# Kernel optimization log

Measured on AMD Instinct MI355X. Metric: run time of the kernel, lower is better.

Reference implementation:

```python
import jax, jax.numpy as jnp
import numpy as np


def setup_inputs() -> dict:
    key = jax.random.key(0)
    k1, k2 = jax.random.split(key)
    B, C, H, W = 64, 512, 28, 28
    x = jax.random.normal(k1, (B, C, H, W), dtype=jnp.float32)
    cc = jax.random.randint(k2, (B, H, W), 0, 2).astype(jnp.bool_)
    return {"x": x, "cc": cc}


def reference(x, cc):
    # x: [B, C, H, W], cc: [B, H, W] bool mask
    m = cc.astype(x.dtype)
    # ave_pool: tmp initialized to x[:, :, 0, 0], then accumulates masked positions
    masked_sum = jnp.einsum('bchw,bhw->bc', x, m) + x[:, :, 0, 0]  # [B, C]
    cnt = jnp.sum(m, axis=(1, 2))                                   # [B]
    denom = jnp.where(cnt == 0, jnp.ones_like(cnt), cnt)            # count==0 -> no division
    mean_pool = masked_sum / denom[:, None]                         # [B, C]
    # AdaptiveMaxPool2d(1): global spatial max
    max_pool = jnp.max(x, axis=(2, 3))                              # [B, C]
    return jnp.concatenate([mean_pool, max_pool], axis=1)           # [B, 2C]
```

## Files before the change

### kernel.cpp

```cpp
#include <hip/hip_runtime.h>


#define HW   784
#define NV4  196
#define NC   512
#define NB   64

__global__ __launch_bounds__(256) void mask_prep_kernel(
    const void* __restrict__ cc, float* __restrict__ mask_f,
    float* __restrict__ invd)
{
    __shared__ float s_cnt;
    __shared__ int s_bad_int, s_bad_flt;
    const int b = blockIdx.x;
    const int t = threadIdx.x;
    if (t == 0) { s_cnt = 0.0f; s_bad_int = 0; s_bad_flt = 0; }
    __syncthreads();

    const int* cci = (const int*)cc;
    if (t < NV4) {
        int v = cci[b * NV4 + t];
        if (v & ~1) atomicOr(&s_bad_int, 1);
        if (v != 0 && v != 0x3F800000) atomicOr(&s_bad_flt, 1);
    }
    __syncthreads();

    float local = 0.0f;
    if (s_bad_int == 0) {
        const int* row = cci + (size_t)b * HW;
        for (int i = t; i < HW; i += 256) {
            float mv = (float)row[i];
            mask_f[b * HW + i] = mv; local += mv;
        }
    } else if (s_bad_flt == 0) {
        const float* row = (const float*)cc + (size_t)b * HW;
        for (int i = t; i < HW; i += 256) {
            float mv = row[i];
            mask_f[b * HW + i] = mv; local += mv;
        }
    } else {
        const unsigned char* row = (const unsigned char*)cc + (size_t)b * HW;
        for (int i = t; i < HW; i += 256) {
            float mv = (float)row[i];
            mask_f[b * HW + i] = mv; local += mv;
        }
    }
    atomicAdd(&s_cnt, local);
    __syncthreads();
    if (t == 0) {
        float c = s_cnt;
        invd[b] = 1.0f / ((c == 0.0f) ? 1.0f : c);
    }
}

__device__ __forceinline__ float dot4(float4 a, float4 b) {
    return a.x * b.x + a.y * b.y + a.z * b.z + a.w * b.w;
}
__device__ __forceinline__ float max4(float4 a) {
    return fmaxf(fmaxf(a.x, a.y), fmaxf(a.z, a.w));
}

__global__ __launch_bounds__(256) void pool_main_kernel(
    const float* __restrict__ x, const float* __restrict__ mask_f,
    const float* __restrict__ invd, float* __restrict__ out)
{
    const int blk  = blockIdx.x;
    const int b    = blk >> 5;
    const int grp  = blk & 31;
    const int t    = threadIdx.x;
    const int wave = t >> 6;
    const int lane = t & 63;
    const int c0   = grp * 16 + wave * 4;

    const float4* m4 = (const float4*)(mask_f + (size_t)b * HW);
    float4 m0 = m4[lane];
    float4 m1 = m4[lane + 64];
    float4 m2 = m4[lane + 128];
    float4 m3 = (lane < 4) ? m4[lane + 192] : make_float4(0.f, 0.f, 0.f, 0.f);
    const float inv = invd[b];

    float s[4], mx[4];
#pragma unroll
    for (int j = 0; j < 4; ++j) {
        const float4* xr = (const float4*)(x + (size_t)(b * NC + c0 + j) * HW);
        float4 q0 = xr[lane];
        float4 q1 = xr[lane + 64];
        float4 q2 = xr[lane + 128];
        float sum = dot4(q0, m0) + dot4(q1, m1) + dot4(q2, m2);
        float mm  = fmaxf(fmaxf(max4(q0), max4(q1)), max4(q2));
        if (lane < 4) {
            float4 q3 = xr[lane + 192];
            sum += dot4(q3, m3);
            mm = fmaxf(mm, max4(q3));
        }
        if (lane == 0) sum += q0.x;
        s[j] = sum; mx[j] = mm;
    }

#pragma unroll
    for (int j = 0; j < 4; ++j) {
        float sum = s[j], mm = mx[j];
        for (int off = 32; off > 0; off >>= 1) {
            sum += __shfl_down(sum, off);
            mm   = fmaxf(mm, __shfl_down(mm, off));
        }
        if (lane == 0) {
            const int c = c0 + j;
            out[(size_t)b * (2 * NC) + c]      = sum * inv;
            out[(size_t)b * (2 * NC) + NC + c] = mm;
        }
    }
}

extern "C" void kernel_launch(void* const* d_in, const int* in_sizes, int n_in,
                              void* d_out, int out_size, void* d_ws, size_t ws_size,
                              hipStream_t stream) {
    const float* x  = (const float*)d_in[0];
    const void*  cc = d_in[1];
    float* out    = (float*)d_out;
    float* mask_f = (float*)d_ws;
    float* invd   = (float*)d_ws + (size_t)NB * HW;

    mask_prep_kernel<<<dim3(NB), dim3(256), 0, stream>>>(cc, mask_f, invd);
    pool_main_kernel<<<dim3(NB * 32), dim3(256), 0, stream>>>(x, mask_f, invd, out);
}
```

Baseline: 155.6 us.

## Fuse mask preparation into pooling kernel and drop separate prep launch

Removes the mask_prep kernel and its workspace round trip. Each wave of the pooling kernel now detects the mask dtype, loads and converts the mask itself, and computes the count and reciprocal locally. The count reduction is interleaved with the per-channel sum and max reductions in one shuffle loop. This removes one launch and the dependency between two kernels, at the cost of every wave redundantly reading and converting the mask.

```diff
diff --git a/kernel.cpp b/kernel.cpp
--- a/kernel.cpp
+++ b/kernel.cpp
@@ -1,57 +1,9 @@
 #include <hip/hip_runtime.h>
 
 
-#define HW   784
-#define NV4  196
-#define NC   512
-#define NB   64
-
-__global__ __launch_bounds__(256) void mask_prep_kernel(
-    const void* __restrict__ cc, float* __restrict__ mask_f,
-    float* __restrict__ invd)
-{
-    __shared__ float s_cnt;
-    __shared__ int s_bad_int, s_bad_flt;
-    const int b = blockIdx.x;
-    const int t = threadIdx.x;
-    if (t == 0) { s_cnt = 0.0f; s_bad_int = 0; s_bad_flt = 0; }
-    __syncthreads();
-
-    const int* cci = (const int*)cc;
-    if (t < NV4) {
-        int v = cci[b * NV4 + t];
-        if (v & ~1) atomicOr(&s_bad_int, 1);
-        if (v != 0 && v != 0x3F800000) atomicOr(&s_bad_flt, 1);
-    }
-    __syncthreads();
-
-    float local = 0.0f;
-    if (s_bad_int == 0) {
-        const int* row = cci + (size_t)b * HW;
-        for (int i = t; i < HW; i += 256) {
-            float mv = (float)row[i];
-            mask_f[b * HW + i] = mv; local += mv;
-        }
-    } else if (s_bad_flt == 0) {
-        const float* row = (const float*)cc + (size_t)b * HW;
-        for (int i = t; i < HW; i += 256) {
-            float mv = row[i];
-            mask_f[b * HW + i] = mv; local += mv;
-        }
-    } else {
-        const unsigned char* row = (const unsigned char*)cc + (size_t)b * HW;
-        for (int i = t; i < HW; i += 256) {
-            float mv = (float)row[i];
-            mask_f[b * HW + i] = mv; local += mv;
-        }
-    }
-    atomicAdd(&s_cnt, local);
-    __syncthreads();
-    if (t == 0) {
-        float c = s_cnt;
-        invd[b] = 1.0f / ((c == 0.0f) ? 1.0f : c);
-    }
-}
+#define HW 784
+#define NC 512
+#define NB 64
 
 __device__ __forceinline__ float dot4(float4 a, float4 b) {
     return a.x * b.x + a.y * b.y + a.z * b.z + a.w * b.w;
@@ -59,10 +11,17 @@
 __device__ __forceinline__ float max4(float4 a) {
     return fmaxf(fmaxf(a.x, a.y), fmaxf(a.z, a.w));
 }
+__device__ __forceinline__ float sum4(float4 a) {
+    return a.x + a.y + a.z + a.w;
+}
+__device__ __forceinline__ float4 unpack_u8(unsigned int u) {
+    return make_float4((float)(u & 0xff), (float)((u >> 8) & 0xff),
+                       (float)((u >> 16) & 0xff), (float)((u >> 24) & 0xff));
+}
 
-__global__ __launch_bounds__(256) void pool_main_kernel(
-    const float* __restrict__ x, const float* __restrict__ mask_f,
-    const float* __restrict__ invd, float* __restrict__ out)
+__global__ __launch_bounds__(256) void pool_fused_kernel(
+    const float* __restrict__ x, const void* __restrict__ cc,
+    float* __restrict__ out)
 {
     const int blk  = blockIdx.x;
     const int b    = blk >> 5;
@@ -72,12 +31,44 @@
     const int lane = t & 63;
     const int c0   = grp * 16 + wave * 4;
 
-    const float4* m4 = (const float4*)(mask_f + (size_t)b * HW);
-    float4 m0 = m4[lane];
-    float4 m1 = m4[lane + 64];
-    float4 m2 = m4[lane + 128];
-    float4 m3 = (lane < 4) ? m4[lane + 192] : make_float4(0.f, 0.f, 0.f, 0.f);
-    const float inv = invd[b];
+    int badInt = 0, badFlt = 0;
+    {
+        const int4* det = (const int4*)((const unsigned char*)cc + (size_t)b * HW);
+        if (lane < 49) {
+            int4 d = det[lane];
+            badInt = (d.x | d.y | d.z | d.w) & ~1;
+            badFlt = (d.x && d.x != 0x3F800000) || (d.y && d.y != 0x3F800000) ||
+                     (d.z && d.z != 0x3F800000) || (d.w && d.w != 0x3F800000);
+        }
+    }
+    const bool isInt = !__any(badInt != 0);
+    const bool isFlt = !__any(badFlt);
+
+    float4 m0, m1, m2, m3 = make_float4(0.f, 0.f, 0.f, 0.f);
+    if (isInt) {
+        const int4* mi = (const int4*)cc + (size_t)b * 196;
+        int4 a = mi[lane], e = mi[lane + 64], f = mi[lane + 128];
+        m0 = make_float4((float)a.x, (float)a.y, (float)a.z, (float)a.w);
+        m1 = make_float4((float)e.x, (float)e.y, (float)e.z, (float)e.w);
+        m2 = make_float4((float)f.x, (float)f.y, (float)f.z, (float)f.w);
+        if (lane < 4) {
+            int4 g = mi[lane + 192];
+            m3 = make_float4((float)g.x, (float)g.y, (float)g.z, (float)g.w);
+        }
+    } else if (isFlt) {
+        const float4* mf = (const float4*)cc + (size_t)b * 196;
+        m0 = mf[lane]; m1 = mf[lane + 64]; m2 = mf[lane + 128];
+        if (lane < 4) m3 = mf[lane + 192];
+    } else {
+        const unsigned int* row =
+            (const unsigned int*)((const unsigned char*)cc + (size_t)b * HW);
+        m0 = unpack_u8(row[lane]);
+        m1 = unpack_u8(row[lane + 64]);
+        m2 = unpack_u8(row[lane + 128]);
+        if (lane < 4) m3 = unpack_u8(row[lane + 192]);
+    }
+
+    float mc = sum4(m0) + sum4(m1) + sum4(m2) + sum4(m3);
 
     float s[4], mx[4];
 #pragma unroll
@@ -97,17 +88,22 @@
         s[j] = sum; mx[j] = mm;
     }
 
+    for (int off = 32; off > 0; off >>= 1) {
+        mc += __shfl_down(mc, off);
 #pragma unroll
-    for (int j = 0; j < 4; ++j) {
-        float sum = s[j], mm = mx[j];
-        for (int off = 32; off > 0; off >>= 1) {
-            sum += __shfl_down(sum, off);
-            mm   = fmaxf(mm, __shfl_down(mm, off));
+        for (int j = 0; j < 4; ++j) {
+            s[j] += __shfl_down(s[j], off);
+            mx[j] = fmaxf(mx[j], __shfl_down(mx[j], off));
         }
-        if (lane == 0) {
+    }
+
+    if (lane == 0) {
+        const float inv = 1.0f / ((mc == 0.0f) ? 1.0f : mc);
+#pragma unroll
+        for (int j = 0; j < 4; ++j) {
             const int c = c0 + j;
-            out[(size_t)b * (2 * NC) + c]      = sum * inv;
-            out[(size_t)b * (2 * NC) + NC + c] = mm;
+            out[(size_t)b * (2 * NC) + c]      = s[j] * inv;
+            out[(size_t)b * (2 * NC) + NC + c] = mx[j];
         }
     }
 }
@@ -117,10 +113,6 @@
                               hipStream_t stream) {
     const float* x  = (const float*)d_in[0];
     const void*  cc = d_in[1];
-    float* out    = (float*)d_out;
-    float* mask_f = (float*)d_ws;
-    float* invd   = (float*)d_ws + (size_t)NB * HW;
-
-    mask_prep_kernel<<<dim3(NB), dim3(256), 0, stream>>>(cc, mask_f, invd);
-    pool_main_kernel<<<dim3(NB * 32), dim3(256), 0, stream>>>(x, mask_f, invd, out);
+    float* out = (float*)d_out;
+    pool_fused_kernel<<<dim3(NB * 32), dim3(256), 0, stream>>>(x, cc, out);
 }
```

Measured after the change: 152.0 us. 2.3% less time.
